# Kernel tuning notes

Measured on AMD Instinct MI355X. Metric: run time of the kernel, lower is better.

The kernel has to match this reference:

```python
import jax, jax.numpy as jnp
import numpy as np


def setup_inputs() -> dict:
    key = jax.random.key(0)
    k1, k2 = jax.random.split(key)
    B, H, W, C = 8, 2048, 2048, 21
    yp = jax.random.randint(k1, (B, H, W), 0, C, dtype=jnp.int32)
    y = jax.random.randint(k2, (B, H, W), 0, C, dtype=jnp.int32)
    res = jnp.zeros((B, C, C), dtype=jnp.float32)
    return {"yp": yp, "y": y, "res": res, "n_classes": C}


def reference(yp, y, res, n_classes):
    # Faithful math of Confusion_Matrix.forward:
    # res[i] = histogram over pixels of (yp*n_classes + y), reshaped [C, C].
    # (The torch scatter trick sets x2[i][idx_j, j] = 1 on a zero buffer and
    #  sums over j -> exactly a bincount of idx; res input is fully overwritten.)
    B = yp.shape[0]
    C = n_classes
    idx = (yp.reshape(B, -1) * C + y.reshape(B, -1))  # [B, N] int32 in [0, C*C)
    hist = jnp.zeros((B, C * C), dtype=jnp.float32)
    hist = hist.at[jnp.arange(B)[:, None], idx].add(1.0)
    return hist.reshape(B, C, C)
```

## Files before the change

kernel.cpp:

```cpp
#include <hip/hip_runtime.h>

constexpr int C  = 21;
constexpr int CC = C * C;
constexpr int NSUB = 4;

__global__ void zero_out_kernel(float* __restrict__ out, int n) {
    int i = blockIdx.x * blockDim.x + threadIdx.x;
    if (i < n) out[i] = 0.0f;
}

__global__ __launch_bounds__(256)
void conf_hist_kernel(const int* __restrict__ yp,
                      const int* __restrict__ y,
                      float* __restrict__ out,
                      int n_per_batch,
                      int blocks_per_batch) {
    __shared__ unsigned int hist[NSUB][CC];

    const int tid = threadIdx.x;

    for (int i = tid; i < NSUB * CC; i += blockDim.x)
        ((unsigned int*)hist)[i] = 0u;
    __syncthreads();

    const int b   = blockIdx.x / blocks_per_batch;
    const int blk = blockIdx.x % blocks_per_batch;

    const int4* yp4 = (const int4*)(yp + (size_t)b * n_per_batch);
    const int4* y4  = (const int4*)(y  + (size_t)b * n_per_batch);
    const int n4 = n_per_batch >> 2;

    const int wave = tid >> 6;
    unsigned int* h = hist[wave];

    for (int i = blk * (int)blockDim.x + tid; i < n4;
         i += blocks_per_batch * (int)blockDim.x) {
        int4 a = yp4[i];
        int4 c = y4[i];
        atomicAdd(&h[a.x * C + c.x], 1u);
        atomicAdd(&h[a.y * C + c.y], 1u);
        atomicAdd(&h[a.z * C + c.z], 1u);
        atomicAdd(&h[a.w * C + c.w], 1u);
    }
    __syncthreads();

    float* ob = out + (size_t)b * CC;
    for (int i = tid; i < CC; i += blockDim.x) {
        unsigned int s = hist[0][i] + hist[1][i] + hist[2][i] + hist[3][i];
        if (s) atomicAdd(&ob[i], (float)s);
    }
}

extern "C" void kernel_launch(void* const* d_in, const int* in_sizes, int n_in,
                              void* d_out, int out_size, void* d_ws, size_t ws_size,
                              hipStream_t stream) {
    const int* yp = (const int*)d_in[0];
    const int* y  = (const int*)d_in[1];
    float* out    = (float*)d_out;

    const int total = in_sizes[0];
    const int B = out_size / CC;
    const int n_per_batch = total / B;

    zero_out_kernel<<<(out_size + 255) / 256, 256, 0, stream>>>(out, out_size);

    const int blocks_per_batch = 256;
    conf_hist_kernel<<<B * blocks_per_batch, 256, 0, stream>>>(
        yp, y, out, n_per_batch, blocks_per_batch);
}
```

Before: 55.35 us.

## Replace global float atomics with per-block partial histograms and a reduce kernel

Each histogram block now writes its merged shared-memory histogram to a workspace buffer, and a second kernel sums the partials per batch, replacing both the zero kernel and the global float atomicAdds. The main loop is also unrolled by two so each thread has two int4 loads of each input in flight. The old atomic path stays as a fallback when the workspace is too small. This adds an extra launch and a serial 256-step reduction per output element, and makes the result deterministic.

```diff
diff --git a/kernel.cpp b/kernel.cpp
--- a/kernel.cpp
+++ b/kernel.cpp
@@ -4,22 +4,16 @@
 constexpr int CC = C * C;
 constexpr int NSUB = 4;
 
-__global__ void zero_out_kernel(float* __restrict__ out, int n) {
-    int i = blockIdx.x * blockDim.x + threadIdx.x;
-    if (i < n) out[i] = 0.0f;
-}
-
 __global__ __launch_bounds__(256)
-void conf_hist_kernel(const int* __restrict__ yp,
-                      const int* __restrict__ y,
-                      float* __restrict__ out,
-                      int n_per_batch,
-                      int blocks_per_batch) {
+void conf_hist_partial(const int* __restrict__ yp,
+                       const int* __restrict__ y,
+                       unsigned int* __restrict__ partial,
+                       int n_per_batch,
+                       int blocks_per_batch) {
     __shared__ unsigned int hist[NSUB][CC];
 
     const int tid = threadIdx.x;
-
-    for (int i = tid; i < NSUB * CC; i += blockDim.x)
+    for (int i = tid; i < NSUB * CC; i += 256)
         ((unsigned int*)hist)[i] = 0u;
     __syncthreads();
 
@@ -29,12 +23,76 @@
     const int4* yp4 = (const int4*)(yp + (size_t)b * n_per_batch);
     const int4* y4  = (const int4*)(y  + (size_t)b * n_per_batch);
     const int n4 = n_per_batch >> 2;
+    const int stride = blocks_per_batch * 256;
 
-    const int wave = tid >> 6;
-    unsigned int* h = hist[wave];
+    unsigned int* h = hist[tid >> 6];
 
-    for (int i = blk * (int)blockDim.x + tid; i < n4;
-         i += blocks_per_batch * (int)blockDim.x) {
+    for (int i0 = blk * 256 + tid; i0 < n4; i0 += 2 * stride) {
+        const int i1 = i0 + stride;
+        int4 a0 = yp4[i0];
+        int4 c0 = y4[i0];
+        int4 a1, c1;
+        const bool has1 = (i1 < n4);
+        if (has1) { a1 = yp4[i1]; c1 = y4[i1]; }
+
+        atomicAdd(&h[a0.x * C + c0.x], 1u);
+        atomicAdd(&h[a0.y * C + c0.y], 1u);
+        atomicAdd(&h[a0.z * C + c0.z], 1u);
+        atomicAdd(&h[a0.w * C + c0.w], 1u);
+        if (has1) {
+            atomicAdd(&h[a1.x * C + c1.x], 1u);
+            atomicAdd(&h[a1.y * C + c1.y], 1u);
+            atomicAdd(&h[a1.z * C + c1.z], 1u);
+            atomicAdd(&h[a1.w * C + c1.w], 1u);
+        }
+    }
+    __syncthreads();
+
+    unsigned int* pb = partial + (size_t)blockIdx.x * CC;
+    for (int i = tid; i < CC; i += 256)
+        pb[i] = hist[0][i] + hist[1][i] + hist[2][i] + hist[3][i];
+}
+
+__global__ __launch_bounds__(512)
+void conf_reduce(const unsigned int* __restrict__ partial,
+                 float* __restrict__ out,
+                 int blocks_per_batch) {
+    const int b = blockIdx.x;
+    const int i = threadIdx.x;
+    if (i < CC) {
+        const unsigned int* p = partial + (size_t)b * blocks_per_batch * CC + i;
+        unsigned int s = 0;
+        for (int k = 0; k < blocks_per_batch; ++k)
+            s += p[(size_t)k * CC];
+        out[(size_t)b * CC + i] = (float)s;
+    }
+}
+
+__global__ void zero_out_kernel(float* __restrict__ out, int n) {
+    int i = blockIdx.x * blockDim.x + threadIdx.x;
+    if (i < n) out[i] = 0.0f;
+}
+
+__global__ __launch_bounds__(256)
+void conf_hist_atomic(const int* __restrict__ yp,
+                      const int* __restrict__ y,
+                      float* __restrict__ out,
+                      int n_per_batch,
+                      int blocks_per_batch) {
+    __shared__ unsigned int hist[NSUB][CC];
+    const int tid = threadIdx.x;
+    for (int i = tid; i < NSUB * CC; i += 256)
+        ((unsigned int*)hist)[i] = 0u;
+    __syncthreads();
+
+    const int b   = blockIdx.x / blocks_per_batch;
+    const int blk = blockIdx.x % blocks_per_batch;
+    const int4* yp4 = (const int4*)(yp + (size_t)b * n_per_batch);
+    const int4* y4  = (const int4*)(y  + (size_t)b * n_per_batch);
+    const int n4 = n_per_batch >> 2;
+    unsigned int* h = hist[tid >> 6];
+
+    for (int i = blk * 256 + tid; i < n4; i += blocks_per_batch * 256) {
         int4 a = yp4[i];
         int4 c = y4[i];
         atomicAdd(&h[a.x * C + c.x], 1u);
@@ -45,7 +103,7 @@
     __syncthreads();
 
     float* ob = out + (size_t)b * CC;
-    for (int i = tid; i < CC; i += blockDim.x) {
+    for (int i = tid; i < CC; i += 256) {
         unsigned int s = hist[0][i] + hist[1][i] + hist[2][i] + hist[3][i];
         if (s) atomicAdd(&ob[i], (float)s);
     }
@@ -62,9 +120,18 @@
     const int B = out_size / CC;
     const int n_per_batch = total / B;
 
-    zero_out_kernel<<<(out_size + 255) / 256, 256, 0, stream>>>(out, out_size);
+    const int blocks_per_batch = 256;
+    const int nblocks = B * blocks_per_batch;
+    const size_t ws_needed = (size_t)nblocks * CC * sizeof(unsigned int);
 
-    const int blocks_per_batch = 256;
-    conf_hist_kernel<<<B * blocks_per_batch, 256, 0, stream>>>(
-        yp, y, out, n_per_batch, blocks_per_batch);
+    if (ws_size >= ws_needed) {
+        unsigned int* partial = (unsigned int*)d_ws;
+        conf_hist_partial<<<nblocks, 256, 0, stream>>>(
+            yp, y, partial, n_per_batch, blocks_per_batch);
+        conf_reduce<<<B, 512, 0, stream>>>(partial, out, blocks_per_batch);
+    } else {
+        zero_out_kernel<<<(out_size + 255) / 256, 256, 0, stream>>>(out, out_size);
+        conf_hist_atomic<<<nblocks, 256, 0, stream>>>(
+            yp, y, out, n_per_batch, blocks_per_batch);
+    }
 }
```

Measured after the change: 79.21 us. 43.1% more time.
